# Kernel tuning notes

Measured on AMD Instinct MI355X. Metric: run time of the kernel, lower is better.

## Reference

```python
import jax, jax.numpy as jnp
import numpy as np

D_MODEL = 1024
NHEAD = 16
HEAD_DIM = D_MODEL // NHEAD
WINDOW = 256


def setup_inputs() -> dict:
    key = jax.random.key(0)
    kx, kq, kk, kv, ko = jax.random.split(key, 5)
    B, S = 2, 2048
    scale = 1.0 / np.sqrt(D_MODEL)
    x = jax.random.normal(kx, (B, S, D_MODEL), dtype=jnp.float32)
    Wq = jax.random.normal(kq, (D_MODEL, D_MODEL), dtype=jnp.float32) * scale
    Wk = jax.random.normal(kk, (D_MODEL, D_MODEL), dtype=jnp.float32) * scale
    Wv = jax.random.normal(kv, (D_MODEL, D_MODEL), dtype=jnp.float32) * scale
    Wo = jax.random.normal(ko, (D_MODEL, D_MODEL), dtype=jnp.float32) * scale
    return {"x": x, "Wq": Wq, "Wk": Wk, "Wv": Wv, "Wo": Wo}


def _sliding_window_mask(seq_len):
    # additive mask: 0 where (q - window + 1) <= k <= q, -inf elsewhere
    pos = jnp.arange(seq_len)
    qpos = pos[:, None]
    kpos = pos[None, :]
    valid = (kpos >= qpos - WINDOW + 1) & (kpos <= qpos)
    return jnp.where(valid, 0.0, -jnp.inf).astype(jnp.float32)


def reference(x, Wq, Wk, Wv, Wo):
    B, S, D = x.shape
    # projections (nn.Linear: x @ W.T; weights here stored as [out,in] equiv -> use x @ W.T)
    q = jnp.einsum('bsd,ed->bse', x, Wq)
    k = jnp.einsum('bsd,ed->bse', x, Wk)
    v = jnp.einsum('bsd,ed->bse', x, Wv)
    q = q.reshape(B, S, NHEAD, HEAD_DIM).transpose(0, 2, 1, 3)  # [B,H,S,Dh]
    k = k.reshape(B, S, NHEAD, HEAD_DIM).transpose(0, 2, 1, 3)
    v = v.reshape(B, S, NHEAD, HEAD_DIM).transpose(0, 2, 1, 3)
    mask = _sliding_window_mask(S)  # [S,S]
    scale = 1.0 / np.sqrt(HEAD_DIM)
    scores = jnp.einsum('bhqd,bhkd->bhqk', q, k) * scale + mask
    attn = jax.nn.softmax(scores, axis=-1)
    out = jnp.einsum('bhqk,bhkd->bhqd', attn, v)  # [B,H,S,Dh]
    out = out.transpose(0, 2, 1, 3).reshape(B, S, D)
    return jnp.einsum('bsd,ed->bse', out, Wo)
```

## Files before the change

kernel.cpp:

```cpp
#include <hip/hip_runtime.h>
#include <stdint.h>

#define S_LEN   2048
#define BATCH   2
#define DM      1024
#define NHEADS  16
#define HD      64
#define WIN     256
#define MROWS   (BATCH * S_LEN)
#define NX      (MROWS * DM)
#define NW      (DM * DM)

typedef unsigned short u16;
typedef unsigned int   u32;

using short8  = __attribute__((ext_vector_type(8))) short;
using floatx4 = __attribute__((ext_vector_type(4))) float;

__device__ __forceinline__ float bf2f(u16 u) {
    union { u32 u; float f; } v; v.u = ((u32)u) << 16; return v.f;
}
__device__ __forceinline__ u16 f2bf(float f) {
    union { float f; u32 u; } v; v.f = f;
    u32 u = v.u;
    u += 0x7fffu + ((u >> 16) & 1u);
    return (u16)(u >> 16);
}

__device__ __forceinline__ void load_lds16(const void* g, void* l) {
    __builtin_amdgcn_global_load_lds(
        (__attribute__((address_space(1))) void*)(uintptr_t)g,
        (__attribute__((address_space(3))) void*)(unsigned int)(uintptr_t)l,
        16, 0, 0);
}

__global__ __launch_bounds__(256) void normalize_inputs(
        const void* x, const void* wq, const void* wk, const void* wv, const void* wo,
        u16* xb, u16* wcat, u16* wob, int* flag) {
    __shared__ int sbad;
    if (threadIdx.x == 0) sbad = 0;
    __syncthreads();
    int bad = 0;
    for (int i = threadIdx.x; i < 4096; i += 256) {
        float v = bf2f(((const u16*)x)[i]);
        if (!(fabsf(v) < 1e6f)) bad = 1;
    }
    if (bad) atomicOr(&sbad, 1);
    __syncthreads();
    const int mode = sbad;
    if (blockIdx.x == 0 && threadIdx.x == 0) flag[0] = mode;
    if (mode == 0) return;
    const int total = NX + 4 * NW;
    for (int i = blockIdx.x * blockDim.x + threadIdx.x; i < total;
         i += gridDim.x * blockDim.x) {
        const void* src; u16* dst; int li;
        if (i < NX)              { src = x;  dst = xb;            li = i; }
        else if (i < NX + NW)    { src = wq; dst = wcat;          li = i - NX; }
        else if (i < NX + 2*NW)  { src = wk; dst = wcat + NW;     li = i - NX - NW; }
        else if (i < NX + 3*NW)  { src = wv; dst = wcat + 2*NW;   li = i - NX - 2*NW; }
        else                     { src = wo; dst = wob;           li = i - NX - 3*NW; }
        dst[li] = f2bf(((const float*)src)[li]);
    }
}

#define BK 32

template<int TBM, int TBN>
__global__ __launch_bounds__(256) void gemm_lds(
        const u16* __restrict__ Araw, const u16* __restrict__ Anorm,
        const u16* __restrict__ B0, const u16* __restrict__ B1,
        const u16* __restrict__ B2, const u16* __restrict__ Bnorm,
        void* __restrict__ C, u16* __restrict__ VT,
        int M, int N, int K,
        const int* __restrict__ flag, int final_out) {
    constexpr int NI = TBM / 32, NF = TBN / 32;
    __shared__ __align__(16) u16 sA[2][TBM * BK];
    __shared__ __align__(16) u16 sB[2][TBN * BK];

    const int mode = flag[0];
    const int tid  = threadIdx.x;
    const int lane = tid & 63, wave = tid >> 6;
    const int m0  = blockIdx.x * TBM;
    const int n0g = blockIdx.y * TBN;
    const int third = n0g >> 10;
    const u16* A = mode ? Anorm : Araw;
    const u16* B = mode ? (Bnorm + (size_t)third * NW)
                        : (third == 0 ? B0 : (third == 1 ? B1 : B2));
    const int n0 = n0g - third * 1024;

    const int srow = lane >> 2;
    const int scol = (lane & 3) * 8;
    const u16* gA = A + (size_t)(m0 + wave * 16 + srow) * K + scol;
    const u16* gB = B + (size_t)(n0 + wave * 16 + srow) * K + scol;
    const size_t rstep = (size_t)64 * K;
    const int lofs = wave * 16 * BK;

    const int n16 = lane & 15, quad = lane >> 4;
    const int m_off = (wave >> 1) * (TBM / 2), n_off = (wave & 1) * (TBN / 2);

    floatx4 acc[NI][NF] = {};
    const int NIT = K / BK;

    auto issue = [&](int k0, int buf) {
        #pragma unroll
        for (int ia = 0; ia < TBM / 64; ++ia)
            load_lds16(gA + k0 + ia * rstep, sA[buf] + lofs + ia * 64 * BK);
        #pragma unroll
        for (int ib = 0; ib < TBN / 64; ++ib)
            load_lds16(gB + k0 + ib * rstep, sB[buf] + lofs + ib * 64 * BK);
    };

    issue(0, 0);
    for (int it = 0; it < NIT; ++it) {
        const int cur = it & 1;
        __syncthreads();
        if (it + 1 < NIT) issue((it + 1) * BK, 1 - cur);
        short8 af[NI], bfr[NF];
        #pragma unroll
        for (int i = 0; i < NI; ++i)
            af[i] = *(const short8*)&sA[cur][(m_off + i * 16 + n16) * BK + quad * 8];
        #pragma unroll
        for (int j = 0; j < NF; ++j)
            bfr[j] = *(const short8*)&sB[cur][(n_off + j * 16 + n16) * BK + quad * 8];
        #pragma unroll
        for (int i = 0; i < NI; ++i) {
            #pragma unroll
            for (int j = 0; j < NF; ++j)
                acc[i][j] = __builtin_amdgcn_mfma_f32_16x16x32_bf16(
                    af[i], bfr[j], acc[i][j], 0, 0, 0);
        }
    }

    if (!final_out && n0g >= 2048) {
        #pragma unroll
        for (int i = 0; i < NI; ++i) {
            #pragma unroll
            for (int j = 0; j < NF; ++j) {
                int row = m0 + m_off + i * 16 + quad * 4;
                int b_ = row >> 11, s = row & 2047;
                int cv = (n0g - 2048) + n_off + j * 16 + n16;
                int h_ = cv >> 6, dl = cv & 63;
                u16 pack[4];
                #pragma unroll
                for (int r = 0; r < 4; ++r) pack[r] = f2bf(acc[i][j][r]);
                u16* dst = VT + (((size_t)(b_ * 16 + h_) * 64 + dl) * S_LEN + s);
                *(uint2*)dst = *(uint2*)pack;
            }
        }
        return;
    }
    const int outmode = final_out ? mode : 0;
    const float oscale = (!final_out && n0g < 1024) ? 0.125f : 1.0f;
    #pragma unroll
    for (int i = 0; i < NI; ++i) {
        #pragma unroll
        for (int j = 0; j < NF; ++j) {
            #pragma unroll
            for (int r = 0; r < 4; ++r) {
                int row = m0 + m_off + i * 16 + quad * 4 + r;
                int col = n0g + n_off + j * 16 + n16;
                size_t idx = (size_t)row * N + col;
                float v = acc[i][j][r] * oscale;
                if (outmode) ((float*)C)[idx] = v;
                else         ((u16*)C)[idx]   = f2bf(v);
            }
        }
    }
}

#define NCHUNK 10

__global__ __launch_bounds__(256) void attn_mfma(
        const u16* __restrict__ QKV, const u16* __restrict__ VT,
        u16* __restrict__ O) {
    __shared__ __align__(16) u16 sK[2][32][72];
    __shared__ __align__(16) u16 sVt[2][64][40];
    __shared__ __align__(16) u16 sP[4][2][16][40];

    const int bh = blockIdx.x;
    const int b  = bh >> 4, h = bh & 15;
    const int q0 = blockIdx.y * 64;
    const int ks0 = q0 - 256;
    const int tid = threadIdx.x;
    const u16* base = QKV + (size_t)b * S_LEN * 3072;
    const u16* Kb = base + 1024 + h * 64;
    const u16* Vb = VT + (size_t)bh * 64 * S_LEN;

    const int kRow = tid >> 3;
    const int kSeg = tid & 7;
    const int vD   = tid >> 2;
    const int vSeg = tid & 3;

    auto stage = [&](int c, int buf) {
        const int ks = ks0 + c * 32;
        int kg = ks + kRow;
        uint4 kv = {0u, 0u, 0u, 0u};
        if (kg >= 0 && kg < S_LEN)
            kv = *(const uint4*)(Kb + (size_t)kg * 3072 + kSeg * 8);
        *(uint4*)&sK[buf][kRow][kSeg * 8] = kv;
        int vk = ks + vSeg * 8;
        uint4 vv = {0u, 0u, 0u, 0u};
        if (vk >= 0 && vk + 8 <= S_LEN)
            vv = *(const uint4*)(Vb + (size_t)vD * S_LEN + vk);
        *(uint4*)&sVt[buf][vD][vSeg * 8] = vv;
    };

    const int wave = tid >> 6, lane = tid & 63;
    const int n16 = lane & 15, quad = lane >> 4;
    const int sqb = q0 + wave * 16;
    const int sq_r0 = sqb + quad * 4;
    const int cfirst = wave >> 1;

    const u16* qrow = base + (size_t)(sqb + n16) * 3072 + h * 64;
    short8 aq0 = *(const short8*)(qrow + quad * 8);
    short8 aq1 = *(const short8*)(qrow + 32 + quad * 8);

    floatx4 o0 = {0.f,0.f,0.f,0.f}, o1 = o0, o2 = o0, o3 = o0;
    float lsum[4] = {0.f, 0.f, 0.f, 0.f};

    stage(0, 0);
    for (int c = 0; c < NCHUNK; ++c) {
        const int buf = c & 1;
        __syncthreads();
        if (c + 1 < NCHUNK) stage(c + 1, 1 - buf);
        if (c < cfirst || c > cfirst + 8) continue;

        short8 bk00 = *(const short8*)&sK[buf][n16][quad * 8];
        short8 bk01 = *(const short8*)&sK[buf][n16][32 + quad * 8];
        short8 bk10 = *(const short8*)&sK[buf][16 + n16][quad * 8];
        short8 bk11 = *(const short8*)&sK[buf][16 + n16][32 + quad * 8];
        floatx4 z = {0.f, 0.f, 0.f, 0.f};
        floatx4 s0 = __builtin_amdgcn_mfma_f32_16x16x32_bf16(aq0, bk00, z, 0, 0, 0);
        s0 = __builtin_amdgcn_mfma_f32_16x16x32_bf16(aq1, bk01, s0, 0, 0, 0);
        floatx4 s1 = __builtin_amdgcn_mfma_f32_16x16x32_bf16(aq0, bk10, z, 0, 0, 0);
        s1 = __builtin_amdgcn_mfma_f32_16x16x32_bf16(aq1, bk11, s1, 0, 0, 0);

        const int kg0 = ks0 + c * 32 + n16;
        const int kg1 = kg0 + 16;
        float p0[4], p1[4];
        #pragma unroll
        for (int r = 0; r < 4; ++r) {
            int sq = sq_r0 + r;
            int lo = sq - (WIN - 1); if (lo < 0) lo = 0;
            float v0 = (kg0 >= lo && kg0 <= sq) ? s0[r] : -3e38f;
            float v1 = (kg1 >= lo && kg1 <= sq) ? s1[r] : -3e38f;
            p0[r] = __expf(v0);
            p1[r] = __expf(v1);
            lsum[r] += p0[r] + p1[r];
        }
        u16* pw = &sP[wave][c & 1][0][0];
        #pragma unroll
        for (int r = 0; r < 4; ++r) {
            pw[(quad * 4 + r) * 40 + n16]      = f2bf(p0[r]);
            pw[(quad * 4 + r) * 40 + 16 + n16] = f2bf(p1[r]);
        }
        asm volatile("s_waitcnt lgkmcnt(0)" ::: "memory");
        short8 pa  = *(const short8*)&pw[n16 * 40 + quad * 8];
        short8 bv0 = *(const short8*)&sVt[buf][n16]     [quad * 8];
        short8 bv1 = *(const short8*)&sVt[buf][16 + n16][quad * 8];
        short8 bv2 = *(const short8*)&sVt[buf][32 + n16][quad * 8];
        short8 bv3 = *(const short8*)&sVt[buf][48 + n16][quad * 8];
        o0 = __builtin_amdgcn_mfma_f32_16x16x32_bf16(pa, bv0, o0, 0, 0, 0);
        o1 = __builtin_amdgcn_mfma_f32_16x16x32_bf16(pa, bv1, o1, 0, 0, 0);
        o2 = __builtin_amdgcn_mfma_f32_16x16x32_bf16(pa, bv2, o2, 0, 0, 0);
        o3 = __builtin_amdgcn_mfma_f32_16x16x32_bf16(pa, bv3, o3, 0, 0, 0);
    }

    #pragma unroll
    for (int r = 0; r < 4; ++r) {
        float s = lsum[r];
        s += __shfl_xor(s, 1);
        s += __shfl_xor(s, 2);
        s += __shfl_xor(s, 4);
        s += __shfl_xor(s, 8);
        lsum[r] = s;
    }

    #pragma unroll
    for (int r = 0; r < 4; ++r) {
        float rl = 1.0f / lsum[r];
        size_t ro = ((size_t)(b * S_LEN + sq_r0 + r)) * DM + h * 64 + n16;
        O[ro]      = f2bf(o0[r] * rl);
        O[ro + 16] = f2bf(o1[r] * rl);
        O[ro + 32] = f2bf(o2[r] * rl);
        O[ro + 48] = f2bf(o3[r] * rl);
    }
}

extern "C" void kernel_launch(void* const* d_in, const int* in_sizes, int n_in,
                              void* d_out, int out_size, void* d_ws, size_t ws_size,
                              hipStream_t stream) {
    char* ws = (char*)d_ws;
    int* flag = (int*)ws;
    u16* xb   = (u16*)(ws + 1024);
    u16* wcat = xb   + (size_t)NX;
    u16* wob  = wcat + (size_t)3 * NW;
    u16* qkv  = wob  + (size_t)NW;
    u16* ob   = qkv  + (size_t)MROWS * 3 * DM;
    u16* vt   = ob   + (size_t)NX;

    const u16* xr  = (const u16*)d_in[0];
    const u16* wqr = (const u16*)d_in[1];
    const u16* wkr = (const u16*)d_in[2];
    const u16* wvr = (const u16*)d_in[3];
    const u16* wor = (const u16*)d_in[4];

    normalize_inputs<<<1024, 256, 0, stream>>>(
        d_in[0], d_in[1], d_in[2], d_in[3], d_in[4], xb, wcat, wob, flag);
    gemm_lds<128, 128><<<dim3(MROWS / 128, 3072 / 128), 256, 0, stream>>>(
        xr, xb, wqr, wkr, wvr, wcat, qkv, vt, MROWS, 3 * DM, DM, flag, 0);
    attn_mfma<<<dim3(BATCH * NHEADS, S_LEN / 64), 256, 0, stream>>>(qkv, vt, ob);
    gemm_lds<64, 64><<<dim3(MROWS / 64, DM / 64), 256, 0, stream>>>(
        ob, ob, wor, wor, wor, wob, d_out, vt, MROWS, DM, DM, flag, 1);
}
```

Measured before the change: 162.6 us.

## Add dedicated 256x256 QKV GEMM with 4-stage LDS pipeline and swizzle

Replaces the generic 128x128 QKV projection GEMM with a specialized kernel. It uses 256x256 tiles, 512 threads, and a 4-deep LDS ring buffer with three K-steps prefetched. A and B stage loads are interleaved with MFMA phases, with manual vmcnt waits, barriers and setprio to overlap loads with compute, and an XOR swizzle to avoid LDS bank conflicts. The larger tile raises operand reuse but reduces the grid to 192 blocks, which may underfill the CUs, and it increases register and LDS pressure.

Result: slower. 167.8 us (+3.2%).

```diff
diff --git a/kernel.cpp b/kernel.cpp
--- a/kernel.cpp
+++ b/kernel.cpp
@@ -63,6 +63,145 @@
     }
 }
 
+#define QBM 256
+#define QBN 256
+#define QBK 32
+#define QNT (DM / QBK)
+
+__global__ __launch_bounds__(512, 2) void gemm_qkv(
+        const u16* __restrict__ Araw, const u16* __restrict__ Anorm,
+        const u16* __restrict__ B0, const u16* __restrict__ B1,
+        const u16* __restrict__ B2, const u16* __restrict__ Bnorm,
+        u16* __restrict__ C, u16* __restrict__ VT,
+        const int* __restrict__ flag) {
+    __shared__ __align__(16) u16 sA[4][QBM * QBK];
+    __shared__ __align__(16) u16 sB[4][QBN * QBK];
+
+    const int mode = flag[0];
+    const int tid  = threadIdx.x;
+    const int lane = tid & 63, wave = tid >> 6;
+    const int n16 = lane & 15, quad = lane >> 4;
+    const int m0  = blockIdx.x * QBM;
+    const int n0g = blockIdx.y * QBN;
+    const int third = n0g >> 10;
+    const u16* A = mode ? Anorm : Araw;
+    const u16* B = mode ? (Bnorm + (size_t)third * NW)
+                        : (third == 0 ? B0 : (third == 1 ? B1 : B2));
+    const int n0 = n0g - third * 1024;
+    const int K = DM;
+
+    const int srow = tid >> 2;
+    const int srb  = ((tid & 3) * 16) ^ (((tid >> 3) & 3) << 4);
+    const u16* gA = A + (size_t)(m0 + srow) * K + (srb >> 1);
+    const u16* gB = B + (size_t)(n0 + srow) * K + (srb >> 1);
+    const size_t rhalf = (size_t)128 * K;
+    const int ldst = wave * 1024;
+
+    auto stageA = [&](int u) {
+        char* base = (char*)&sA[u & 3][0] + ldst;
+        const u16* g = gA + u * QBK;
+        load_lds16(g,         base);
+        load_lds16(g + rhalf, base + 8192);
+    };
+    auto stageB = [&](int u) {
+        char* base = (char*)&sB[u & 3][0] + ldst;
+        const u16* g = gB + u * QBK;
+        load_lds16(g,         base);
+        load_lds16(g + rhalf, base + 8192);
+    };
+
+    const int wm0 = (wave >> 2) * 128;
+    const int wn0 = (wave & 3) * 64;
+    const int rsw = ((n16 >> 1) & 3) << 4;
+    const int cb  = (quad * 16) ^ rsw;
+    const int aoff = (wm0 + n16) * 32 + (cb >> 1);
+    const int boff = (wn0 + n16) * 32 + (cb >> 1);
+
+    stageA(0); stageB(0);
+    stageA(1); stageB(1);
+    stageA(2); stageB(2);
+    asm volatile("s_waitcnt vmcnt(8)" ::: "memory");
+    __builtin_amdgcn_s_barrier();
+    __builtin_amdgcn_sched_barrier(0);
+
+    floatx4 acc[8][4] = {};
+
+    for (int t = 0; t < QNT; ++t) {
+        const u16* sAb = sA[t & 3];
+        const u16* sBb = sB[t & 3];
+
+        short8 af[8], b0, b1;
+        #pragma unroll
+        for (int i = 0; i < 8; ++i)
+            af[i] = *(const short8*)&sAb[aoff + i * 512];
+        b0 = *(const short8*)&sBb[boff];
+        b1 = *(const short8*)&sBb[boff + 512];
+        if (t + 3 < QNT) stageA(t + 3);
+        __builtin_amdgcn_s_barrier();
+        __builtin_amdgcn_s_setprio(1);
+        #pragma unroll
+        for (int i = 0; i < 8; ++i)
+            acc[i][0] = __builtin_amdgcn_mfma_f32_16x16x32_bf16(af[i], b0, acc[i][0], 0, 0, 0);
+        #pragma unroll
+        for (int i = 0; i < 8; ++i)
+            acc[i][1] = __builtin_amdgcn_mfma_f32_16x16x32_bf16(af[i], b1, acc[i][1], 0, 0, 0);
+        __builtin_amdgcn_s_setprio(0);
+        __builtin_amdgcn_s_barrier();
+
+        b0 = *(const short8*)&sBb[boff + 1024];
+        b1 = *(const short8*)&sBb[boff + 1536];
+        if (t + 3 < QNT) stageB(t + 3);
+        __builtin_amdgcn_s_barrier();
+        __builtin_amdgcn_s_setprio(1);
+        #pragma unroll
+        for (int i = 0; i < 8; ++i)
+            acc[i][2] = __builtin_amdgcn_mfma_f32_16x16x32_bf16(af[i], b0, acc[i][2], 0, 0, 0);
+        #pragma unroll
+        for (int i = 0; i < 8; ++i)
+            acc[i][3] = __builtin_amdgcn_mfma_f32_16x16x32_bf16(af[i], b1, acc[i][3], 0, 0, 0);
+        __builtin_amdgcn_s_setprio(0);
+
+        __builtin_amdgcn_sched_barrier(0);
+        if (t < QNT - 3)       asm volatile("s_waitcnt vmcnt(8)" ::: "memory");
+        else if (t == QNT - 3) asm volatile("s_waitcnt vmcnt(4)" ::: "memory");
+        else if (t == QNT - 2) asm volatile("s_waitcnt vmcnt(0)" ::: "memory");
+        __builtin_amdgcn_s_barrier();
+        __builtin_amdgcn_sched_barrier(0);
+    }
+
+    if (n0g >= 2048) {
+        #pragma unroll
+        for (int i = 0; i < 8; ++i) {
+            #pragma unroll
+            for (int j = 0; j < 4; ++j) {
+                int row = m0 + wm0 + i * 16 + quad * 4;
+                int b_ = row >> 11, s = row & 2047;
+                int cv = (n0g - 2048) + wn0 + j * 16 + n16;
+                int h_ = cv >> 6, dl = cv & 63;
+                u16 pack[4];
+                #pragma unroll
+                for (int r = 0; r < 4; ++r) pack[r] = f2bf(acc[i][j][r]);
+                u16* dst = VT + (((size_t)(b_ * 16 + h_) * 64 + dl) * S_LEN + s);
+                *(uint2*)dst = *(uint2*)pack;
+            }
+        }
+        return;
+    }
+    const float oscale = (n0g < 1024) ? 0.125f : 1.0f;
+    #pragma unroll
+    for (int i = 0; i < 8; ++i) {
+        #pragma unroll
+        for (int j = 0; j < 4; ++j) {
+            #pragma unroll
+            for (int r = 0; r < 4; ++r) {
+                int row = m0 + wm0 + i * 16 + quad * 4 + r;
+                int col = n0g + wn0 + j * 16 + n16;
+                C[(size_t)row * 3072 + col] = f2bf(acc[i][j][r] * oscale);
+            }
+        }
+    }
+}
+
 #define BK 32
 
 template<int TBM, int TBN>
@@ -131,24 +270,6 @@
         }
     }
 
-    if (!final_out && n0g >= 2048) {
-        #pragma unroll
-        for (int i = 0; i < NI; ++i) {
-            #pragma unroll
-            for (int j = 0; j < NF; ++j) {
-                int row = m0 + m_off + i * 16 + quad * 4;
-                int b_ = row >> 11, s = row & 2047;
-                int cv = (n0g - 2048) + n_off + j * 16 + n16;
-                int h_ = cv >> 6, dl = cv & 63;
-                u16 pack[4];
-                #pragma unroll
-                for (int r = 0; r < 4; ++r) pack[r] = f2bf(acc[i][j][r]);
-                u16* dst = VT + (((size_t)(b_ * 16 + h_) * 64 + dl) * S_LEN + s);
-                *(uint2*)dst = *(uint2*)pack;
-            }
-        }
-        return;
-    }
     const int outmode = final_out ? mode : 0;
     const float oscale = (!final_out && n0g < 1024) ? 0.125f : 1.0f;
     #pragma unroll
@@ -307,8 +428,8 @@
 
     normalize_inputs<<<1024, 256, 0, stream>>>(
         d_in[0], d_in[1], d_in[2], d_in[3], d_in[4], xb, wcat, wob, flag);
-    gemm_lds<128, 128><<<dim3(MROWS / 128, 3072 / 128), 256, 0, stream>>>(
-        xr, xb, wqr, wkr, wvr, wcat, qkv, vt, MROWS, 3 * DM, DM, flag, 0);
+    gemm_qkv<<<dim3(MROWS / 256, 3072 / 256), 512, 0, stream>>>(
+        xr, xb, wqr, wkr, wvr, wcat, qkv, vt, flag);
     attn_mfma<<<dim3(BATCH * NHEADS, S_LEN / 64), 256, 0, stream>>>(qkv, vt, ob);
     gemm_lds<64, 64><<<dim3(MROWS / 64, DM / 64), 256, 0, stream>>>(
         ob, ob, wor, wor, wor, wob, d_out, vt, MROWS, DM, DM, flag, 1);
```
